# Performance work log

Hardware: AMD Instinct MI355X
Metric: run time of the kernel (lower is better)

The kernel has to match this reference:

```python
import jax, jax.numpy as jnp
import numpy as np

N_NODES = 100000
N_EDGES = 500000
IN_DIM, HID, N_CLS = 128, 512, 40


def gcn_conv(x, W, b, src, dst, num_nodes):
    # PyG GCNConv: h = x W; add self-loops; norm = d^-1/2[src] * d^-1/2[dst];
    # out[dst] += norm * h[src]; out += bias
    h = x @ W  # [N, out_dim]
    ones = jnp.ones(src.shape[0], dtype=x.dtype)
    deg = jax.ops.segment_sum(ones, dst, num_segments=num_nodes)  # in-degree incl self-loops
    dinv = jnp.where(deg > 0, jax.lax.rsqrt(deg), 0.0)
    norm = dinv[src] * dinv[dst]  # [E]
    msgs = h[src] * norm[:, None]  # [E, out_dim] gather + scale
    out = jax.ops.segment_sum(msgs, dst, num_segments=num_nodes)
    return out + b


def setup_inputs() -> dict:
    key = jax.random.key(0)
    k1, k2, k3, k4, k5, k6 = jax.random.split(key, 6)
    x = jax.random.normal(k1, (N_NODES, IN_DIM), dtype=jnp.float32)
    edge_index = jax.random.randint(k2, (2, N_EDGES), 0, N_NODES, dtype=jnp.int32)
    # Glorot-ish params
    W1 = jax.random.normal(k3, (IN_DIM, HID), dtype=jnp.float32) * (1.0 / np.sqrt(IN_DIM))
    b1 = jnp.zeros((HID,), dtype=jnp.float32)
    W2 = jax.random.normal(k4, (HID, N_CLS), dtype=jnp.float32) * (1.0 / np.sqrt(HID))
    b2 = jnp.zeros((N_CLS,), dtype=jnp.float32)
    return {"x": x, "edge_index": edge_index, "W1": W1, "b1": b1, "W2": W2, "b2": b2}


def reference(x, edge_index, W1, b1, W2, b2):
    n = x.shape[0]
    # add self-loops once, shared by both conv layers
    loop = jnp.arange(n, dtype=edge_index.dtype)
    src = jnp.concatenate([edge_index[0], loop])
    dst = jnp.concatenate([edge_index[1], loop])
    h = gcn_conv(x, W1, b1, src, dst, n)
    h = jax.nn.relu(h)
    # dropout is identity in eval mode (reference computed in eval)
    h = gcn_conv(h, W2, b2, src, dst, n)
    return jax.nn.log_softmax(h, axis=1)
```

## Files before the change

kernel.cpp:

```cpp
#include <hip/hip_runtime.h>
#include <cstdint>
#include <cstddef>

#define N_NODES 100000
#define N_EDGES 500000
#define IN_DIM  128
#define HID     512
#define N_CLS   40
#define N_SBLK  ((N_NODES + 255) / 256)
#define N_CNTB  ((N_EDGES + 255) / 256)
#define N_XBFB  12500
#define N_PREPB 352

typedef short bf16x8 __attribute__((ext_vector_type(8)));
typedef float f32x4 __attribute__((ext_vector_type(4)));

__device__ inline unsigned short f2bf(float f) {
  unsigned u = __float_as_uint(f);
  u = u + 0x7fffu + ((u >> 16) & 1u);
  return (unsigned short)(u >> 16);
}
__device__ inline float blo(unsigned u) { return __uint_as_float(u << 16); }
__device__ inline float bhi(unsigned u) { return __uint_as_float(u & 0xffff0000u); }

__global__ __launch_bounds__(256) void k_zero(int* __restrict__ cnt, unsigned* __restrict__ flags) {
  int i = blockIdx.x * 256 + threadIdx.x;
  if (i < N_NODES) cnt[i] = 0;
  if (i < 512) flags[i] = 0;
}

__global__ __launch_bounds__(256) void k_count_xbf(const int* __restrict__ dst, int* __restrict__ cnt,
                                                   const float* __restrict__ x, uint2* __restrict__ xb2) {
  int b = blockIdx.x;
  if (b < N_CNTB) {
    int e = b * 256 + threadIdx.x;
    if (e < N_EDGES) atomicAdd(&cnt[dst[e]], 1);
  } else {
    int t = (b - N_CNTB) * 256 + threadIdx.x;
    float4 v = ((const float4*)x)[t];
    uint2 o;
    o.x = (unsigned)f2bf(v.x) | ((unsigned)f2bf(v.y) << 16);
    o.y = (unsigned)f2bf(v.z) | ((unsigned)f2bf(v.w) << 16);
    xb2[t] = o;
  }
}

__global__ __launch_bounds__(256) void k_scan_prep(const int* __restrict__ cnt, unsigned* __restrict__ flags,
                                                   int* __restrict__ offsets, int* __restrict__ cursor,
                                                   float* __restrict__ dinv,
                                                   const float* __restrict__ W1, const float* __restrict__ W2,
                                                   unsigned short* __restrict__ W1F, unsigned short* __restrict__ W2F) {
  int b = blockIdx.x;
  if (b < N_SBLK) {
    __shared__ int s[256];
    __shared__ int base_sh;
    int i = b * 256 + threadIdx.x;
    int v = (i < N_NODES) ? cnt[i] : 0;
    s[threadIdx.x] = v;
    __syncthreads();
    #pragma unroll
    for (int off = 1; off < 256; off <<= 1) {
      int t = (threadIdx.x >= off) ? s[threadIdx.x - off] : 0;
      __syncthreads();
      s[threadIdx.x] += t;
      __syncthreads();
    }
    int incl = s[threadIdx.x];
    if (threadIdx.x == 0) {
      int total = s[255];
      if (b == 0) {
        atomicExch(&flags[0], (2u << 30) | (unsigned)total);
        base_sh = 0;
      } else {
        atomicExch(&flags[b], (1u << 30) | (unsigned)total);
        int base = 0, pred = b - 1;
        while (true) {
          unsigned f;
          do { f = atomicAdd(&flags[pred], 0u); } while ((f >> 30) == 0u);
          base += (int)(f & 0x3fffffffu);
          if ((f >> 30) == 2u) break;
          --pred;
        }
        atomicExch(&flags[b], (2u << 30) | (unsigned)(base + (unsigned)total));
        base_sh = base;
      }
    }
    __syncthreads();
    int gbase = base_sh;
    if (i < N_NODES) {
      int excl = gbase + incl - v;
      offsets[i] = excl;
      cursor[i]  = excl;
      dinv[i]    = rsqrtf((float)(v + 1));
    }
    if (b == 0 && threadIdx.x == 0) offsets[N_NODES] = N_EDGES;
  } else {
    int t = (b - N_SBLK) * 256 + threadIdx.x;
    if (t < 65536) {
      int j = t & 7, lane = (t >> 3) & 63, rest = t >> 9;
      int s2 = rest & 3, c = rest >> 2;
      int k = s2 * 32 + (lane >> 4) * 8 + j;
      int n = c * 16 + (lane & 15);
      W1F[t] = f2bf(W1[k * HID + n]);
    } else {
      int u = t - 65536;
      int j = u & 7, lane = (u >> 3) & 63, rest = u >> 9;
      int ct = rest % 3, gk = rest / 3;
      int k = gk * 32 + (lane >> 4) * 8 + j;
      int col = ct * 16 + (lane & 15);
      W2F[u] = (col < N_CLS) ? f2bf(W2[k * N_CLS + col]) : (unsigned short)0;
    }
  }
}

__global__ __launch_bounds__(256) void k_fill(const int* __restrict__ src, const int* __restrict__ dst,
                                              const float* __restrict__ dinv,
                                              int* __restrict__ cursor, int2* __restrict__ epair) {
  int e = blockIdx.x * 256 + threadIdx.x;
  if (e >= N_EDGES) return;
  int s = src[e], d = dst[e];
  int pos = atomicAdd(&cursor[d], 1);
  float nrm = dinv[s] * dinv[d];
  epair[pos] = make_int2(s, __float_as_int(nrm));
}

__global__ __launch_bounds__(256) void k_gather1(const uint2* __restrict__ xb, const int2* __restrict__ ep,
                                                 const int* __restrict__ offsets,
                                                 const float* __restrict__ dinv, uint2* __restrict__ z1) {
  int lane = threadIdx.x & 63, h = lane >> 5, l = lane & 31;
  int d = blockIdx.x * 8 + (threadIdx.x >> 6) * 2 + h;
  int start = offsets[d], end = offsets[d + 1];
  float dd = dinv[d], sl = dd * dd;
  uint2 su = xb[(size_t)d * 32 + l];
  float a0 = sl * blo(su.x), a1 = sl * bhi(su.x), a2 = sl * blo(su.y), a3 = sl * bhi(su.y);
  float p0a = 0.f, p1a = 0.f, p2a = 0.f, p3a = 0.f;
  float q0a = 0.f, q1a = 0.f, q2a = 0.f, q3a = 0.f;
  float r0a = 0.f, r1a = 0.f, r2a = 0.f, r3a = 0.f;

  int i = start;
  for (; i + 3 < end; i += 4) {
    int2 e0 = ep[i], e1 = ep[i + 1], e2 = ep[i + 2], e3 = ep[i + 3];
    uint2 r0 = xb[(size_t)e0.x * 32 + l];
    uint2 r1 = xb[(size_t)e1.x * 32 + l];
    uint2 r2 = xb[(size_t)e2.x * 32 + l];
    uint2 r3 = xb[(size_t)e3.x * 32 + l];
    float n0 = __int_as_float(e0.y), n1 = __int_as_float(e1.y);
    float n2 = __int_as_float(e2.y), n3 = __int_as_float(e3.y);
    a0  += n0 * blo(r0.x); a1  += n0 * bhi(r0.x); a2  += n0 * blo(r0.y); a3  += n0 * bhi(r0.y);
    p0a += n1 * blo(r1.x); p1a += n1 * bhi(r1.x); p2a += n1 * blo(r1.y); p3a += n1 * bhi(r1.y);
    q0a += n2 * blo(r2.x); q1a += n2 * bhi(r2.x); q2a += n2 * blo(r2.y); q3a += n2 * bhi(r2.y);
    r0a += n3 * blo(r3.x); r1a += n3 * bhi(r3.x); r2a += n3 * blo(r3.y); r3a += n3 * bhi(r3.y);
  }
  for (; i < end; ++i) {
    int2 e0 = ep[i];
    uint2 r0 = xb[(size_t)e0.x * 32 + l];
    float n0 = __int_as_float(e0.y);
    a0 += n0 * blo(r0.x); a1 += n0 * bhi(r0.x); a2 += n0 * blo(r0.y); a3 += n0 * bhi(r0.y);
  }
  a0 += p0a + q0a + r0a;
  a1 += p1a + q1a + r1a;
  a2 += p2a + q2a + r2a;
  a3 += p3a + q3a + r3a;
  uint2 o;
  o.x = (unsigned)f2bf(a0) | ((unsigned)f2bf(a1) << 16);
  o.y = (unsigned)f2bf(a2) | ((unsigned)f2bf(a3) << 16);
  z1[(size_t)d * 32 + l] = o;
}

#define HS_STRIDE 56
__global__ __launch_bounds__(256) void k_fused_mfma(const unsigned short* __restrict__ z1b,
                                                    const unsigned short* __restrict__ W1F,
                                                    const float* __restrict__ b1,
                                                    const unsigned short* __restrict__ W2F,
                                                    unsigned short* __restrict__ Pb) {
  __shared__ unsigned short Hs[4][64 * HS_STRIDE];
  const int tid  = threadIdx.x;
  const int w    = tid >> 6, lane = tid & 63;
  const int c16  = lane & 15, quad = lane >> 4;
  const int mbase = blockIdx.x * 256 + w * 64;

  bf16x8 afrag[4][4];
  #pragma unroll
  for (int t = 0; t < 4; ++t) {
    int mrow = mbase + t * 16 + c16;
    int meff = (mrow < N_NODES) ? mrow : 0;
    const bf16x8* arow = (const bf16x8*)(z1b + (size_t)meff * IN_DIM + quad * 8);
    afrag[t][0] = arow[0];
    afrag[t][1] = arow[4];
    afrag[t][2] = arow[8];
    afrag[t][3] = arow[12];
  }

  f32x4 pacc[4][3];
  #pragma unroll
  for (int t = 0; t < 4; ++t)
    #pragma unroll
    for (int ct = 0; ct < 3; ++ct) pacc[t][ct] = (f32x4){0.f, 0.f, 0.f, 0.f};

  const bf16x8* w1f = (const bf16x8*)W1F;
  const bf16x8* w2f = (const bf16x8*)W2F;
  unsigned short* hs = Hs[w];

  for (int g = 0; g < 16; ++g) {
    #pragma unroll
    for (int nt = 0; nt < 2; ++nt) {
      int c = g * 2 + nt;
      bf16x8 bp0 = w1f[(c * 4 + 0) * 64 + lane];
      bf16x8 bp1 = w1f[(c * 4 + 1) * 64 + lane];
      bf16x8 bp2 = w1f[(c * 4 + 2) * 64 + lane];
      bf16x8 bp3 = w1f[(c * 4 + 3) * 64 + lane];
      f32x4 h[4];
      #pragma unroll
      for (int t = 0; t < 4; ++t) h[t] = (f32x4){0.f, 0.f, 0.f, 0.f};
      #pragma unroll
      for (int t = 0; t < 4; ++t) h[t] = __builtin_amdgcn_mfma_f32_16x16x32_bf16(afrag[t][0], bp0, h[t], 0, 0, 0);
      #pragma unroll
      for (int t = 0; t < 4; ++t) h[t] = __builtin_amdgcn_mfma_f32_16x16x32_bf16(afrag[t][1], bp1, h[t], 0, 0, 0);
      #pragma unroll
      for (int t = 0; t < 4; ++t) h[t] = __builtin_amdgcn_mfma_f32_16x16x32_bf16(afrag[t][2], bp2, h[t], 0, 0, 0);
      #pragma unroll
      for (int t = 0; t < 4; ++t) h[t] = __builtin_amdgcn_mfma_f32_16x16x32_bf16(afrag[t][3], bp3, h[t], 0, 0, 0);
      float bias = b1[c * 16 + c16];
      #pragma unroll
      for (int t = 0; t < 4; ++t)
        #pragma unroll
        for (int r = 0; r < 4; ++r)
          hs[(t * 16 + quad * 4 + r) * HS_STRIDE + nt * 16 + c16] = f2bf(fmaxf(h[t][r] + bias, 0.f));
    }
    bf16x8 hf[4];
    #pragma unroll
    for (int t = 0; t < 4; ++t)
      hf[t] = *(const bf16x8*)(hs + (t * 16 + c16) * HS_STRIDE + quad * 8);
    #pragma unroll
    for (int ct = 0; ct < 3; ++ct) {
      bf16x8 bf = w2f[(g * 3 + ct) * 64 + lane];
      #pragma unroll
      for (int t = 0; t < 4; ++t)
        pacc[t][ct] = __builtin_amdgcn_mfma_f32_16x16x32_bf16(hf[t], bf, pacc[t][ct], 0, 0, 0);
    }
  }

  #pragma unroll
  for (int t = 0; t < 4; ++t) {
    int mrow0 = mbase + t * 16 + quad * 4;
    #pragma unroll
    for (int ct = 0; ct < 3; ++ct) {
      int col = ct * 16 + c16;
      if (col < N_CLS) {
        #pragma unroll
        for (int r = 0; r < 4; ++r) {
          int m = mrow0 + r;
          if (m < N_NODES) Pb[(size_t)m * N_CLS + col] = f2bf(pacc[t][ct][r]);
        }
      }
    }
  }
}

__global__ __launch_bounds__(256) void k_gather2_lsm(const uint2* __restrict__ Pu2,
                                                     const int2* __restrict__ ep,
                                                     const int* __restrict__ offsets,
                                                     const float* __restrict__ dinv, const float* __restrict__ b2,
                                                     float* __restrict__ out) {
  int lane = threadIdx.x & 63, q = lane >> 4, l = lane & 15;
  int d = blockIdx.x * 16 + (threadIdx.x >> 6) * 4 + q;
  bool act = l < 10;
  int lc = act ? l : 0;
  int start = offsets[d], end = offsets[d + 1];
  float dd = dinv[d], sl = dd * dd;

  uint2 su = Pu2[(size_t)d * 10 + lc];
  float a0 = sl * blo(su.x), a1 = sl * bhi(su.x), a2 = sl * blo(su.y), a3 = sl * bhi(su.y);
  float p0a = 0.f, p1a = 0.f, p2a = 0.f, p3a = 0.f;
  float q0a = 0.f, q1a = 0.f, q2a = 0.f, q3a = 0.f;
  float r0a = 0.f, r1a = 0.f, r2a = 0.f, r3a = 0.f;

  int i = start;
  for (; i + 3 < end; i += 4) {
    int2 e0 = ep[i], e1 = ep[i + 1], e2 = ep[i + 2], e3 = ep[i + 3];
    uint2 u0 = Pu2[(size_t)e0.x * 10 + lc];
    uint2 u1 = Pu2[(size_t)e1.x * 10 + lc];
    uint2 u2 = Pu2[(size_t)e2.x * 10 + lc];
    uint2 u3 = Pu2[(size_t)e3.x * 10 + lc];
    float n0 = __int_as_float(e0.y), n1 = __int_as_float(e1.y);
    float n2 = __int_as_float(e2.y), n3 = __int_as_float(e3.y);
    a0  += n0 * blo(u0.x); a1  += n0 * bhi(u0.x); a2  += n0 * blo(u0.y); a3  += n0 * bhi(u0.y);
    p0a += n1 * blo(u1.x); p1a += n1 * bhi(u1.x); p2a += n1 * blo(u1.y); p3a += n1 * bhi(u1.y);
    q0a += n2 * blo(u2.x); q1a += n2 * bhi(u2.x); q2a += n2 * blo(u2.y); q3a += n2 * bhi(u2.y);
    r0a += n3 * blo(u3.x); r1a += n3 * bhi(u3.x); r2a += n3 * blo(u3.y); r3a += n3 * bhi(u3.y);
  }
  for (; i < end; ++i) {
    int2 e0 = ep[i];
    uint2 u0 = Pu2[(size_t)e0.x * 10 + lc];
    float n0 = __int_as_float(e0.y);
    a0 += n0 * blo(u0.x); a1 += n0 * bhi(u0.x); a2 += n0 * blo(u0.y); a3 += n0 * bhi(u0.y);
  }

  float v0, v1, v2, v3;
  if (act) {
    float4 bb = ((const float4*)b2)[l];
    v0 = a0 + p0a + q0a + r0a + bb.x;
    v1 = a1 + p1a + q1a + r1a + bb.y;
    v2 = a2 + p2a + q2a + r2a + bb.z;
    v3 = a3 + p3a + q3a + r3a + bb.w;
  } else {
    v0 = v1 = v2 = v3 = -1e30f;
  }
  float m = fmaxf(fmaxf(v0, v1), fmaxf(v2, v3));
  #pragma unroll
  for (int off = 8; off > 0; off >>= 1) m = fmaxf(m, __shfl_xor(m, off, 64));
  float e = act ? (expf(v0 - m) + expf(v1 - m) + expf(v2 - m) + expf(v3 - m)) : 0.f;
  float s = e;
  #pragma unroll
  for (int off = 8; off > 0; off >>= 1) s += __shfl_xor(s, off, 64);
  float lse = m + logf(s);
  if (act) {
    float4 o = make_float4(v0 - lse, v1 - lse, v2 - lse, v3 - lse);
    ((float4*)(out + (size_t)d * N_CLS))[l] = o;
  }
}

extern "C" void kernel_launch(void* const* d_in, const int* in_sizes, int n_in,
                              void* d_out, int out_size, void* d_ws, size_t ws_size,
                              hipStream_t stream) {
  const float* x  = (const float*)d_in[0];
  const int*   ei = (const int*)d_in[1];
  const int*  src = ei;
  const int*  dst = ei + N_EDGES;
  const float* W1 = (const float*)d_in[2];
  const float* b1 = (const float*)d_in[3];
  const float* W2 = (const float*)d_in[4];
  const float* b2 = (const float*)d_in[5];
  float* out = (float*)d_out;

  float* dinv    = (float*)d_ws;
  int*   cnt     = (int*)(dinv + 131072);
  int*   offsets = cnt + 131072;
  int*   cursor  = offsets + 131072;
  unsigned* flags = (unsigned*)(cursor + 131072);
  int2*  epair   = (int2*)(flags + 1024);
  uint2* xb2     = (uint2*)(epair + 524288);
  unsigned short* Pb = (unsigned short*)xb2;
  unsigned short* z1b = (unsigned short*)(xb2 + 3200000);
  unsigned short* W1F = z1b + (size_t)N_NODES * IN_DIM;
  unsigned short* W2F = W1F + HID * IN_DIM;

  k_zero <<<(N_NODES + 255) / 256, 256, 0, stream>>>(cnt, flags);
  k_count_xbf<<<N_CNTB + N_XBFB, 256, 0, stream>>>(dst, cnt, x, xb2);
  k_scan_prep<<<N_SBLK + N_PREPB, 256, 0, stream>>>(cnt, flags, offsets, cursor, dinv, W1, W2, W1F, W2F);
  k_fill <<<N_CNTB, 256, 0, stream>>>(src, dst, dinv, cursor, epair);
  k_gather1<<<N_NODES / 8, 256, 0, stream>>>(xb2, epair, offsets, dinv, (uint2*)z1b);
  k_fused_mfma<<<(N_NODES + 255) / 256, 256, 0, stream>>>(z1b, W1F, b1, W2F, Pb);
  k_gather2_lsm<<<N_NODES / 16, 256, 0, stream>>>((const uint2*)Pb, epair, offsets, dinv, b2, out);
}
```

Before: 246.1 us.

## Merge graph-build kernels into one persistent kernel; shrink MFMA blocks and pack bf16 stores

Replaces the count/convert, scan/prep and fill kernels with a single persistent kernel that uses grid-stride loops and two global atomic barriers, removing two launches and the gaps between them. The fused MFMA kernel moves to 64-thread blocks (one wave per block) and writes the ReLU output as packed bf16 pairs using a lane shuffle and v_cvt_pk_bf16_f32, which halves the LDS store count. The grid barriers assume all 743 blocks are co-resident, so the kernel can deadlock if occupancy is lower than expected. The scan's decoupled look-back also now runs inside that barrier-synchronized kernel.

```diff
diff --git a/kernel.cpp b/kernel.cpp
--- a/kernel.cpp
+++ b/kernel.cpp
@@ -8,9 +8,10 @@
 #define HID     512
 #define N_CLS   40
 #define N_SBLK  ((N_NODES + 255) / 256)
-#define N_CNTB  ((N_EDGES + 255) / 256)
-#define N_XBFB  12500
 #define N_PREPB 352
+#define N_BUILD (N_SBLK + N_PREPB)
+#define BUILD_THREADS (N_BUILD * 256)
+#define XBF_TOTAL 3200000
 
 typedef short bf16x8 __attribute__((ext_vector_type(8)));
 typedef float f32x4 __attribute__((ext_vector_type(4)));
@@ -26,47 +27,53 @@
 __global__ __launch_bounds__(256) void k_zero(int* __restrict__ cnt, unsigned* __restrict__ flags) {
   int i = blockIdx.x * 256 + threadIdx.x;
   if (i < N_NODES) cnt[i] = 0;
-  if (i < 512) flags[i] = 0;
-}
-
-__global__ __launch_bounds__(256) void k_count_xbf(const int* __restrict__ dst, int* __restrict__ cnt,
-                                                   const float* __restrict__ x, uint2* __restrict__ xb2) {
-  int b = blockIdx.x;
-  if (b < N_CNTB) {
-    int e = b * 256 + threadIdx.x;
-    if (e < N_EDGES) atomicAdd(&cnt[dst[e]], 1);
-  } else {
-    int t = (b - N_CNTB) * 256 + threadIdx.x;
+  if (i < 1024) flags[i] = 0;
+}
+
+__global__ __launch_bounds__(256, 4) void k_build(const int* __restrict__ src, const int* __restrict__ dst,
+                                                  int* __restrict__ cnt, unsigned* __restrict__ flags,
+                                                  int* __restrict__ offsets, int* __restrict__ cursor,
+                                                  float* __restrict__ dinv,
+                                                  const float* __restrict__ x, uint2* __restrict__ xb2,
+                                                  const float* __restrict__ W1, const float* __restrict__ W2,
+                                                  unsigned short* __restrict__ W1F, unsigned short* __restrict__ W2F,
+                                                  int2* __restrict__ epair) {
+  __shared__ int s[256];
+  __shared__ int base_sh;
+  const int b = blockIdx.x, tid = threadIdx.x;
+  const int gt = b * 256 + tid;
+
+  for (int e = gt; e < N_EDGES; e += BUILD_THREADS) atomicAdd(&cnt[dst[e]], 1);
+  __threadfence();
+  __syncthreads();
+  if (tid == 0) atomicAdd(&flags[512], 1u);
+
+  for (int t = gt; t < XBF_TOTAL; t += BUILD_THREADS) {
     float4 v = ((const float4*)x)[t];
     uint2 o;
     o.x = (unsigned)f2bf(v.x) | ((unsigned)f2bf(v.y) << 16);
     o.y = (unsigned)f2bf(v.z) | ((unsigned)f2bf(v.w) << 16);
     xb2[t] = o;
   }
-}
-
-__global__ __launch_bounds__(256) void k_scan_prep(const int* __restrict__ cnt, unsigned* __restrict__ flags,
-                                                   int* __restrict__ offsets, int* __restrict__ cursor,
-                                                   float* __restrict__ dinv,
-                                                   const float* __restrict__ W1, const float* __restrict__ W2,
-                                                   unsigned short* __restrict__ W1F, unsigned short* __restrict__ W2F) {
-  int b = blockIdx.x;
+
+  if (tid == 0) { while (atomicAdd(&flags[512], 0u) < (unsigned)N_BUILD) __builtin_amdgcn_s_sleep(2); }
+  __syncthreads();
+  __threadfence();
+
   if (b < N_SBLK) {
-    __shared__ int s[256];
-    __shared__ int base_sh;
-    int i = b * 256 + threadIdx.x;
+    int i = b * 256 + tid;
     int v = (i < N_NODES) ? cnt[i] : 0;
-    s[threadIdx.x] = v;
+    s[tid] = v;
     __syncthreads();
     #pragma unroll
     for (int off = 1; off < 256; off <<= 1) {
-      int t = (threadIdx.x >= off) ? s[threadIdx.x - off] : 0;
+      int t = (tid >= off) ? s[tid - off] : 0;
       __syncthreads();
-      s[threadIdx.x] += t;
+      s[tid] += t;
       __syncthreads();
     }
-    int incl = s[threadIdx.x];
-    if (threadIdx.x == 0) {
+    int incl = s[tid];
+    if (tid == 0) {
       int total = s[255];
       if (b == 0) {
         atomicExch(&flags[0], (2u << 30) | (unsigned)total);
@@ -93,9 +100,9 @@
       cursor[i]  = excl;
       dinv[i]    = rsqrtf((float)(v + 1));
     }
-    if (b == 0 && threadIdx.x == 0) offsets[N_NODES] = N_EDGES;
+    if (b == 0 && tid == 0) offsets[N_NODES] = N_EDGES;
   } else {
-    int t = (b - N_SBLK) * 256 + threadIdx.x;
+    int t = (b - N_SBLK) * 256 + tid;
     if (t < 65536) {
       int j = t & 7, lane = (t >> 3) & 63, rest = t >> 9;
       int s2 = rest & 3, c = rest >> 2;
@@ -111,17 +118,21 @@
       W2F[u] = (col < N_CLS) ? f2bf(W2[k * N_CLS + col]) : (unsigned short)0;
     }
   }
-}
-
-__global__ __launch_bounds__(256) void k_fill(const int* __restrict__ src, const int* __restrict__ dst,
-                                              const float* __restrict__ dinv,
-                                              int* __restrict__ cursor, int2* __restrict__ epair) {
-  int e = blockIdx.x * 256 + threadIdx.x;
-  if (e >= N_EDGES) return;
-  int s = src[e], d = dst[e];
-  int pos = atomicAdd(&cursor[d], 1);
-  float nrm = dinv[s] * dinv[d];
-  epair[pos] = make_int2(s, __float_as_int(nrm));
+  __threadfence();
+  __syncthreads();
+  if (tid == 0) {
+    atomicAdd(&flags[513], 1u);
+    while (atomicAdd(&flags[513], 0u) < (unsigned)N_BUILD) __builtin_amdgcn_s_sleep(2);
+  }
+  __syncthreads();
+  __threadfence();
+
+  for (int e = gt; e < N_EDGES; e += BUILD_THREADS) {
+    int ss = src[e], d = dst[e];
+    int pos = atomicAdd(&cursor[d], 1);
+    float nrm = dinv[ss] * dinv[d];
+    epair[pos] = make_int2(ss, __float_as_int(nrm));
+  }
 }
 
 __global__ __launch_bounds__(256) void k_gather1(const uint2* __restrict__ xb, const int2* __restrict__ ep,
@@ -168,16 +179,16 @@
 }
 
 #define HS_STRIDE 56
-__global__ __launch_bounds__(256) void k_fused_mfma(const unsigned short* __restrict__ z1b,
-                                                    const unsigned short* __restrict__ W1F,
-                                                    const float* __restrict__ b1,
-                                                    const unsigned short* __restrict__ W2F,
-                                                    unsigned short* __restrict__ Pb) {
-  __shared__ unsigned short Hs[4][64 * HS_STRIDE];
-  const int tid  = threadIdx.x;
-  const int w    = tid >> 6, lane = tid & 63;
+__global__ __launch_bounds__(64) void k_fused_mfma(const unsigned short* __restrict__ z1b,
+                                                   const unsigned short* __restrict__ W1F,
+                                                   const float* __restrict__ b1,
+                                                   const unsigned short* __restrict__ W2F,
+                                                   unsigned short* __restrict__ Pb) {
+  __shared__ unsigned short Hs[64 * HS_STRIDE];
+  const int lane = threadIdx.x;
   const int c16  = lane & 15, quad = lane >> 4;
-  const int mbase = blockIdx.x * 256 + w * 64;
+  const int odd  = c16 & 1;
+  const int mbase = blockIdx.x * 64;
 
   bf16x8 afrag[4][4];
   #pragma unroll
@@ -199,7 +210,7 @@
 
   const bf16x8* w1f = (const bf16x8*)W1F;
   const bf16x8* w2f = (const bf16x8*)W2F;
-  unsigned short* hs = Hs[w];
+  unsigned short* hs = Hs;
 
   for (int g = 0; g < 16; ++g) {
     #pragma unroll
@@ -221,11 +232,26 @@
       #pragma unroll
       for (int t = 0; t < 4; ++t) h[t] = __builtin_amdgcn_mfma_f32_16x16x32_bf16(afrag[t][3], bp3, h[t], 0, 0, 0);
       float bias = b1[c * 16 + c16];
-      #pragma unroll
-      for (int t = 0; t < 4; ++t)
-        #pragma unroll
-        for (int r = 0; r < 4; ++r)
-          hs[(t * 16 + quad * 4 + r) * HS_STRIDE + nt * 16 + c16] = f2bf(fmaxf(h[t][r] + bias, 0.f));
+      int colb = nt * 16 + (c16 & ~1);
+      int rb0  = quad * 4 + (odd ? 2 : 0);
+      #pragma unroll
+      for (int t = 0; t < 4; ++t) {
+        float v0 = fmaxf(h[t][0] + bias, 0.f);
+        float v1 = fmaxf(h[t][1] + bias, 0.f);
+        float v2 = fmaxf(h[t][2] + bias, 0.f);
+        float v3 = fmaxf(h[t][3] + bias, 0.f);
+        float o0 = __shfl_xor(v0, 1, 64);
+        float o1 = __shfl_xor(v1, 1, 64);
+        float o2 = __shfl_xor(v2, 1, 64);
+        float o3 = __shfl_xor(v3, 1, 64);
+        float lo0 = odd ? o2 : v0, hi0 = odd ? v2 : o0;
+        float lo1 = odd ? o3 : v1, hi1 = odd ? v3 : o1;
+        unsigned p0, p1;
+        asm("v_cvt_pk_bf16_f32 %0, %1, %2" : "=v"(p0) : "v"(lo0), "v"(hi0));
+        asm("v_cvt_pk_bf16_f32 %0, %1, %2" : "=v"(p1) : "v"(lo1), "v"(hi1));
+        *(unsigned*)(hs + (t * 16 + rb0    ) * HS_STRIDE + colb) = p0;
+        *(unsigned*)(hs + (t * 16 + rb0 + 1) * HS_STRIDE + colb) = p1;
+      }
     }
     bf16x8 hf[4];
     #pragma unroll
@@ -346,10 +372,9 @@
   unsigned short* W2F = W1F + HID * IN_DIM;
 
   k_zero <<<(N_NODES + 255) / 256, 256, 0, stream>>>(cnt, flags);
-  k_count_xbf<<<N_CNTB + N_XBFB, 256, 0, stream>>>(dst, cnt, x, xb2);
-  k_scan_prep<<<N_SBLK + N_PREPB, 256, 0, stream>>>(cnt, flags, offsets, cursor, dinv, W1, W2, W1F, W2F);
-  k_fill <<<N_CNTB, 256, 0, stream>>>(src, dst, dinv, cursor, epair);
+  k_build<<<N_BUILD, 256, 0, stream>>>(src, dst, cnt, flags, offsets, cursor, dinv,
+                                       x, xb2, W1, W2, W1F, W2F, epair);
   k_gather1<<<N_NODES / 8, 256, 0, stream>>>(xb2, epair, offsets, dinv, (uint2*)z1b);
-  k_fused_mfma<<<(N_NODES + 255) / 256, 256, 0, stream>>>(z1b, W1F, b1, W2F, Pb);
+  k_fused_mfma<<<(N_NODES + 63) / 64, 64, 0, stream>>>(z1b, W1F, b1, W2F, Pb);
   k_gather2_lsm<<<N_NODES / 16, 256, 0, stream>>>((const uint2*)Pb, epair, offsets, dinv, b2, out);
 }
```

Result: slower. 523.1 us (+112.5%).
